# Kernel tuning notes

Hardware: AMD Instinct MI355X
Metric: run time of the kernel (lower is better)

Reference implementation:

```python
import jax, jax.numpy as jnp
import numpy as np

# ---- static config (mirrors init_kwargs) ----
B, T, N, FIN = 32, 12, 500, 2
U, ND, ED = 32, 32, 2            # factor dim, node_dim, edge_dim
NRES, NDIL, NSKIP, NEND, NPRED = 32, 32, 256, 512, 12
NBLOCKS, NLAYERS, KS, ORDER = 4, 2, 2, 2
L = NBLOCKS * NLAYERS
DILATIONS = [2 ** i for _ in range(NBLOCKS) for i in range(NLAYERS)]
RF = NBLOCKS * (KS - 1) * (2 ** NLAYERS - 1) + 1  # receptive field = 13
GCIN = (ORDER * ED + 1) * NDIL                     # graph-conv concat channels = 160
BN_EPS = 1e-5


def conv1x1(x, w, b):
    # x: [B,C,N,T], w: [O,C]
    return jnp.einsum('bcnt,oc->bont', x, w) + b[None, :, None, None]


def dilated_tconv(x, w, b, d):
    # valid dilated conv along time. x: [B,C,N,T], w: [O,C,K]
    k_sz = w.shape[-1]
    t_out = x.shape[-1] - (k_sz - 1) * d
    out = jnp.einsum('bcnt,oc->bont', x[..., 0:t_out], w[..., 0])
    for k in range(1, k_sz):
        out = out + jnp.einsum('bcnt,oc->bont', x[..., k * d:k * d + t_out], w[..., k])
    return out + b[None, :, None, None]


def graph_conv(x, supports, w, b):
    # x: [B,C,N,T]; supports: [E,N,N]; diffusion over node axis (dim 2)
    out = [x]
    for e in range(supports.shape[0]):
        x1 = jnp.einsum('bcvt,vw->bcwt', x, supports[e])
        out.append(x1)
        for _ in range(ORDER - 1):
            x1 = jnp.einsum('bcvt,vw->bcwt', x1, supports[e])
            out.append(x1)
    h = jnp.concatenate(out, axis=1)  # [B,GCIN,N,T]
    return conv1x1(h, w, b)


def batchnorm(x, g, bta):
    m = x.mean(axis=(0, 2, 3), keepdims=True)
    v = ((x - m) ** 2).mean(axis=(0, 2, 3), keepdims=True)
    return (x - m) * jax.lax.rsqrt(v + BN_EPS) * g[None, :, None, None] + bta[None, :, None, None]


def _forward(inputs, factor, map_w, map_b, a1w, a1b, a2w, a2b, a3w, a3b,
             enter_w, enter_b, filt_w, filt_b, gate_w, gate_b,
             skp_w, skp_b, gc_w, gc_b, bn_g, bn_b, o1w, o1b, o2w, o2b):
    n = factor.shape[0]
    # ---- adaptive supports ----
    v = jax.nn.relu(factor @ map_w + map_b)                      # [N, ND]
    src = jnp.broadcast_to(v[None, :, :], (n, n, v.shape[1]))    # src[i,j]=v[j]
    dst = jnp.broadcast_to(v[:, None, :], (n, n, v.shape[1]))    # dst[i,j]=v[i]
    h = jnp.concatenate([src, dst], axis=-1)                     # [N,N,2*ND]
    h = jax.nn.relu(h @ a1w + a1b)
    h = jax.nn.relu(h @ a2w + a2b)
    adj = (h @ a3w + a3b).transpose(2, 0, 1)                     # [E,N,N]
    adj = jax.nn.softmax(adj, axis=2)
    supports = jnp.maximum(adj, jnp.eye(n, dtype=adj.dtype))
    # ---- input split ----
    static = jnp.einsum('btuf,pu->btpf', jnp.einsum('btnf,nu->btuf', inputs, factor), factor)
    x = jnp.concatenate([static, inputs - static], axis=-1)      # [B,T,N,2F]
    x = x.transpose(0, 3, 2, 1)                                  # [B,2F,N,T]
    t_in = x.shape[-1]
    if t_in < RF:
        x = jnp.pad(x, ((0, 0), (0, 0), (0, 0), (RF - t_in, 0)))
    x = conv1x1(x, enter_w, enter_b)                             # [B,NRES,N,RF]
    skip = jnp.zeros((x.shape[0], NSKIP, n, x.shape[-1]), dtype=x.dtype)
    # ---- stacked ST layers ----
    for i, d in enumerate(DILATIONS):
        residual = x
        f = jnp.tanh(dilated_tconv(x, filt_w[i], filt_b[i], d))
        g = jax.nn.sigmoid(dilated_tconv(x, gate_w[i], gate_b[i], d))
        x = f * g                                                # [B,NDIL,N,T']
        s = conv1x1(x, skp_w[i], skp_b[i])
        skip = skip[..., skip.shape[-1] - s.shape[-1]:] + s
        x = graph_conv(x, supports, gc_w[i], gc_b[i])
        x = x + residual[..., residual.shape[-1] - x.shape[-1]:]
        x = batchnorm(x, bn_g[i], bn_b[i])
    # ---- output head ----
    y = jax.nn.relu(skip)
    y = jax.nn.relu(conv1x1(y, o1w, o1b))
    y = conv1x1(y, o2w, o2b)                                     # [B,NPRED,N,1]
    return y, supports


def setup_inputs() -> dict:
    key = jax.random.key(0)
    ks = jax.random.split(key, 16)
    def w(i, shape, s=0.02):
        return s * jax.random.normal(ks[i], shape, dtype=jnp.float32)
    return {
        'inputs': jax.random.normal(ks[0], (B, T, N, FIN), dtype=jnp.float32),
        'factor': 0.05 * jax.random.normal(ks[1], (N, U), dtype=jnp.float32),
        'map_w': w(2, (U, ND), 0.1), 'map_b': jnp.zeros((ND,), jnp.float32),
        'a1w': w(3, (2 * ND, 2 * ND), 0.1), 'a1b': jnp.zeros((2 * ND,), jnp.float32),
        'a2w': w(4, (2 * ND, ND), 0.1), 'a2b': jnp.zeros((ND,), jnp.float32),
        'a3w': w(5, (ND, ED), 0.1), 'a3b': jnp.zeros((ED,), jnp.float32),
        'enter_w': w(6, (NRES, 2 * FIN)), 'enter_b': jnp.zeros((NRES,), jnp.float32),
        'filt_w': w(7, (L, NDIL, NRES, KS)), 'filt_b': jnp.zeros((L, NDIL), jnp.float32),
        'gate_w': w(8, (L, NDIL, NRES, KS)), 'gate_b': jnp.zeros((L, NDIL), jnp.float32),
        'skp_w': w(9, (L, NSKIP, NDIL)), 'skp_b': jnp.zeros((L, NSKIP), jnp.float32),
        'gc_w': w(10, (L, NRES, GCIN)), 'gc_b': jnp.zeros((L, NRES), jnp.float32),
        'bn_g': jnp.ones((L, NRES), jnp.float32), 'bn_b': jnp.zeros((L, NRES), jnp.float32),
        'o1w': w(11, (NEND, NSKIP)), 'o1b': jnp.zeros((NEND,), jnp.float32),
        'o2w': w(12, (NPRED, NEND)), 'o2b': jnp.zeros((NPRED,), jnp.float32),
    }


def reference(inputs, factor, map_w, map_b, a1w, a1b, a2w, a2b, a3w, a3b,
              enter_w, enter_b, filt_w, filt_b, gate_w, gate_b,
              skp_w, skp_b, gc_w, gc_b, bn_g, bn_b, o1w, o1b, o2w, o2b):
    return _forward(inputs, factor, map_w, map_b, a1w, a1b, a2w, a2b, a3w, a3b,
                    enter_w, enter_b, filt_w, filt_b, gate_w, gate_b,
                    skp_w, skp_b, gc_w, gc_b, bn_g, bn_b, o1w, o1b, o2w, o2b)
```

## Files before the change

kernel.cpp:

```cpp
#include <hip/hip_runtime.h>
#include <math.h>

#define BB 32
#define TT 12
#define NN 500
#define UU 32
#define CC 32
#define NSKIPC 256
#define NENDC 512
#define NPREDC 12
#define TX 13
#define TG 12
#define QS 384
#define VS 512
#define BNN (BB*NN)
#define DSZ (BNN*TG*CC)
#define BN_EPS 1e-5f

#define OFF_V      0u
#define OFF_ADJ    16000u
#define OFF_ASRC   516000u
#define OFF_ADST   548000u
#define OFF_PROJ   580000u
#define OFF_STAT   582048u
#define OFF_PART   582560u
#define OFF_BSUM   774560u
#define OFF_X      774816u
#define OFF_XN     7430816u
#define OFF_D      14086816u
#define OFF_GBF    38662816u
#define OFF_GLB    41734816u
#define OFF_GT     43782816u
#define OFF_ST     46928544u
#define OFF_SB     47190688u
#define OFF_ST2    47452832u
#define OFF_WSTB   47714976u
#define OFF_O1WB   47747744u
#define OFF_SKV    47813280u
#define OFF_Y1B    49861280u

typedef __attribute__((ext_vector_type(8))) short bf16x8;
typedef __attribute__((ext_vector_type(4))) float f32x4;

__device__ inline unsigned short f2bf(float f) {
  union { float f; unsigned u; } x; x.f = f;
  unsigned r = x.u + 0x7FFFu + ((x.u >> 16) & 1u);
  return (unsigned short)(r >> 16);
}
__device__ inline float bf2f(short s) {
  union { float f; unsigned u; } x;
  x.u = ((unsigned)(unsigned short)s) << 16;
  return x.f;
}
__device__ inline int pk2(float a, float b) {
  return (int)((unsigned)f2bf(a) | ((unsigned)f2bf(b) << 16));
}
__device__ inline bf16x8 pack8(f32x4 a, f32x4 b) {
  union { int i[4]; bf16x8 v; } u;
  u.i[0]=pk2(a.x,a.y); u.i[1]=pk2(a.z,a.w);
  u.i[2]=pk2(b.x,b.y); u.i[3]=pk2(b.z,b.w);
  return u.v;
}
__device__ inline f32x4 reluadd(f32x4 a, f32x4 b) {
  f32x4 r;
  r.x=fmaxf(a.x+b.x,0.f); r.y=fmaxf(a.y+b.y,0.f);
  r.z=fmaxf(a.z+b.z,0.f); r.w=fmaxf(a.w+b.w,0.f);
  return r;
}


__global__ void k_v(const float* __restrict__ factor, const float* __restrict__ map_w,
                    const float* __restrict__ map_b, float* __restrict__ v) {
  int n = blockIdx.x; int d = threadIdx.x;
  __shared__ float fr[UU];
  fr[d] = factor[n*UU + d];
  __syncthreads();
  float acc = map_b[d];
#pragma unroll
  for (int u=0;u<UU;u++) acc += fr[u]*map_w[u*32+d];
  v[n*32+d] = fmaxf(acc, 0.f);
}

__global__ void k_asrc2(const float* __restrict__ v, const float* __restrict__ a1w,
                        const float* __restrict__ a1b,
                        float* __restrict__ asrc, float* __restrict__ adst) {
  int n = blockIdx.x; int o = threadIdx.x;
  __shared__ float vn[32];
  if (o < 32) vn[o] = v[n*32+o];
  __syncthreads();
  float s = 0.f, dst = a1b[o];
#pragma unroll
  for (int u=0;u<32;u++){ s += vn[u]*a1w[u*64+o]; dst += vn[u]*a1w[(32+u)*64+o]; }
  asrc[n*64+o] = s;
  adst[n*64+o] = dst;
}

__global__ __launch_bounds__(256) void k_pair3(const float* __restrict__ asrc,
    const float* __restrict__ adst, const float* __restrict__ a2w,
    const float* __restrict__ a2b, const float* __restrict__ a3w,
    const float* __restrict__ a3b, float* __restrict__ adj) {
  int i = blockIdx.x;
  int tid = threadIdx.x;
  int wid = tid>>6, lane = tid&63;
  int lm = lane&15, g = lane>>4, lk8 = g*8;
  int jb = blockIdx.y*256 + wid*64;
  bf16x8 wf[2][2];
#pragma unroll
  for (int ks=0;ks<2;ks++)
#pragma unroll
    for (int nh=0;nh<2;nh++){
      int n = nh*16+lm;
      f32x4 lo, hi;
      lo.x=a2w[(ks*32+lk8+0)*32+n]; lo.y=a2w[(ks*32+lk8+1)*32+n];
      lo.z=a2w[(ks*32+lk8+2)*32+n]; lo.w=a2w[(ks*32+lk8+3)*32+n];
      hi.x=a2w[(ks*32+lk8+4)*32+n]; hi.y=a2w[(ks*32+lk8+5)*32+n];
      hi.z=a2w[(ks*32+lk8+6)*32+n]; hi.w=a2w[(ks*32+lk8+7)*32+n];
      wf[ks][nh] = pack8(lo, hi);
    }
  float b20 = a2b[lm], b21 = a2b[16+lm];
  float w3e0n0 = a3w[lm*2],      w3e1n0 = a3w[lm*2+1];
  float w3e0n1 = a3w[(16+lm)*2], w3e1n1 = a3w[(16+lm)*2+1];
  float b30 = a3b[0], b31 = a3b[1];
  const float* dp = adst + i*64;
  f32x4 d00 = *(const f32x4*)(dp + lk8);
  f32x4 d01 = *(const f32x4*)(dp + lk8 + 4);
  f32x4 d10 = *(const f32x4*)(dp + 32 + lk8);
  f32x4 d11 = *(const f32x4*)(dp + 32 + lk8 + 4);
#pragma unroll
  for (int mg=0; mg<4; mg++){
    int j = jb + mg*16 + lm;
    int jc = j < 500 ? j : 0;
    const float* ap = asrc + jc*64;
    f32x4 s00=*(const f32x4*)(ap+lk8),    s01=*(const f32x4*)(ap+lk8+4);
    f32x4 s10=*(const f32x4*)(ap+32+lk8), s11=*(const f32x4*)(ap+32+lk8+4);
    bf16x8 a0 = pack8(reluadd(s00,d00), reluadd(s01,d01));
    bf16x8 a1 = pack8(reluadd(s10,d10), reluadd(s11,d11));
    f32x4 acc0 = {b20,b20,b20,b20};
    f32x4 acc1 = {b21,b21,b21,b21};
    acc0 = __builtin_amdgcn_mfma_f32_16x16x32_bf16(a0, wf[0][0], acc0, 0,0,0);
    acc0 = __builtin_amdgcn_mfma_f32_16x16x32_bf16(a1, wf[1][0], acc0, 0,0,0);
    acc1 = __builtin_amdgcn_mfma_f32_16x16x32_bf16(a0, wf[0][1], acc1, 0,0,0);
    acc1 = __builtin_amdgcn_mfma_f32_16x16x32_bf16(a1, wf[1][1], acc1, 0,0,0);
    float e0[4], e1[4];
#pragma unroll
    for (int r=0;r<4;r++){
      float h2a = fmaxf(acc0[r],0.f), h2b = fmaxf(acc1[r],0.f);
      e0[r] = h2a*w3e0n0 + h2b*w3e0n1;
      e1[r] = h2a*w3e1n0 + h2b*w3e1n1;
    }
#pragma unroll
    for (int off=1; off<16; off<<=1){
#pragma unroll
      for (int r=0;r<4;r++){ e0[r]+=__shfl_xor(e0[r],off); e1[r]+=__shfl_xor(e1[r],off); }
    }
    if (lm==0){
      int j4 = jb + mg*16 + g*4;
      if (j4 < 500){
        f32x4 v0={e0[0]+b30,e0[1]+b30,e0[2]+b30,e0[3]+b30};
        f32x4 v1={e1[0]+b31,e1[1]+b31,e1[2]+b31,e1[3]+b31};
        *(f32x4*)(adj + i*500 + j4) = v0;
        *(f32x4*)(adj + 250000 + i*500 + j4) = v1;
      }
    }
  }
}

__global__ __launch_bounds__(256) void k_softmax(const float* __restrict__ adj,
    float* __restrict__ sup_out) {
  int row = blockIdx.x;
  int e = row/NN, i = row%NN;
  const float* a = adj + e*250000 + i*NN;
  __shared__ float red[64];
  float m = -1e30f;
  for (int j=threadIdx.x;j<NN;j+=256) m = fmaxf(m, a[j]);
#pragma unroll
  for (int off=32; off; off>>=1) m = fmaxf(m, __shfl_down(m, off));
  int lane = threadIdx.x & 63, wid = threadIdx.x >> 6;
  if (lane==0) red[wid]=m;
  __syncthreads();
  if (threadIdx.x==0){ float mm=red[0]; for(int w=1;w<4;w++) mm=fmaxf(mm,red[w]); red[32]=mm; }
  __syncthreads();
  m = red[32];
  float s=0.f;
  for (int j=threadIdx.x;j<NN;j+=256) s += __expf(a[j]-m);
#pragma unroll
  for (int off=32; off; off>>=1) s += __shfl_down(s, off);
  if (lane==0) red[wid]=s;
  __syncthreads();
  if (threadIdx.x==0){ float ss=0; for(int w=0;w<4;w++) ss+=red[w]; red[33]=ss; }
  __syncthreads();
  float inv = 1.f/red[33];
  for (int j=threadIdx.x;j<NN;j+=256) {
    float val = __expf(a[j]-m)*inv;
    if (j==i) val = 1.f;
    sup_out[e*250000 + i*NN + j] = val;
  }
}

__global__ __launch_bounds__(256) void k_tposeS(const float* __restrict__ sup,
    short* __restrict__ ST, short* __restrict__ SB) {
  __shared__ float ts[64][68];
  int e = blockIdx.z;
  int v0 = blockIdx.x*64, w0 = blockIdx.y*64;
  int tid = threadIdx.x;
  int vv = tid>>2, wc = (tid&3)*16;
  bool vok = (v0+vv) < 500;
#pragma unroll
  for (int c=0;c<4;c++){
    f32x4 val = {0,0,0,0};
    int wg = w0 + wc + c*4;
    if (vok && wg < 500) val = *(const f32x4*)(sup + e*250000 + (size_t)(v0+vv)*500 + wg);
    *(f32x4*)&ts[vv][wc + c*4] = val;
    int2 pv; pv.x = pk2(val.x, val.y); pv.y = pk2(val.z, val.w);
    *(int2*)(SB + (size_t)e*(512*512) + (size_t)(v0+vv)*VS + wg) = pv;
  }
  __syncthreads();
  int w = tid>>2, vc = (tid&3)*16;
  unsigned short u[16];
#pragma unroll
  for (int j=0;j<16;j++) u[j] = f2bf(ts[vc+j][w]);
  int4 o0, o1;
  o0.x = u[0]|(u[1]<<16);  o0.y = u[2]|(u[3]<<16);
  o0.z = u[4]|(u[5]<<16);  o0.w = u[6]|(u[7]<<16);
  o1.x = u[8]|(u[9]<<16);  o1.y = u[10]|(u[11]<<16);
  o1.z = u[12]|(u[13]<<16); o1.w = u[14]|(u[15]<<16);
  short* op = ST + (size_t)e*(512*512) + (size_t)(w0+w)*VS + v0 + vc;
  *(int4*)(op) = o0;
  *(int4*)(op+8) = o1;
}

__global__ __launch_bounds__(256) void k_ssq(const short* __restrict__ SB,
    const short* __restrict__ ST, short* __restrict__ ST2) {
  __shared__ __align__(16) short As[64*72];
  __shared__ __align__(16) short Bs[64*72];
  int e = blockIdx.z;
  int u0 = blockIdx.x*64, w0 = blockIdx.y*64;
  const short* Ab = SB + (size_t)e*(512*512);
  const short* Bb = ST + (size_t)e*(512*512);
  int tid = threadIdx.x;
  int row = tid>>2, col = (tid&3)*16;
  const short* ap = Ab + (size_t)(u0+row)*VS + col;
  const short* bp = Bb + (size_t)(w0+row)*VS + col;
  f32x4 ra0 = *(const f32x4*)(ap);
  f32x4 ra1 = *(const f32x4*)(ap+8);
  f32x4 rb0 = *(const f32x4*)(bp);
  f32x4 rb1 = *(const f32x4*)(bp+8);
  int wid = tid>>6, lane = tid&63;
  int wr = wid>>1, wc = wid&1;
  int lm = lane&15, lk = (lane>>4)*8;
  f32x4 acc[2][2] = {};
  short* aw = As + row*72 + col;
  short* bw = Bs + row*72 + col;
  for (int kk=0; kk<8; kk++) {
    __syncthreads();
    *(f32x4*)(aw) = ra0; *(f32x4*)(aw+8) = ra1;
    *(f32x4*)(bw) = rb0; *(f32x4*)(bw+8) = rb1;
    __syncthreads();
    if (kk < 7) {
      const short* ap2 = ap + (kk+1)*64;
      const short* bp2 = bp + (kk+1)*64;
      ra0 = *(const f32x4*)(ap2); ra1 = *(const f32x4*)(ap2+8);
      rb0 = *(const f32x4*)(bp2); rb1 = *(const f32x4*)(bp2+8);
    }
#pragma unroll
    for (int ks=0; ks<2; ks++) {
      bf16x8 af0 = *(const bf16x8*)(As + (wr*32 + lm)*72 + ks*32 + lk);
      bf16x8 af1 = *(const bf16x8*)(As + (wr*32 + 16 + lm)*72 + ks*32 + lk);
      bf16x8 bq0 = *(const bf16x8*)(Bs + (wc*32 + lm)*72 + ks*32 + lk);
      bf16x8 bq1 = *(const bf16x8*)(Bs + (wc*32 + 16 + lm)*72 + ks*32 + lk);
      acc[0][0] = __builtin_amdgcn_mfma_f32_16x16x32_bf16(af0, bq0, acc[0][0], 0,0,0);
      acc[0][1] = __builtin_amdgcn_mfma_f32_16x16x32_bf16(af0, bq1, acc[0][1], 0,0,0);
      acc[1][0] = __builtin_amdgcn_mfma_f32_16x16x32_bf16(af1, bq0, acc[1][0], 0,0,0);
      acc[1][1] = __builtin_amdgcn_mfma_f32_16x16x32_bf16(af1, bq1, acc[1][1], 0,0,0);
    }
  }
#pragma unroll
  for (int fm=0; fm<2; fm++) {
    int u4 = u0 + wr*32 + fm*16 + (lane>>4)*4;
#pragma unroll
    for (int fn=0; fn<2; fn++) {
      int w = w0 + wc*32 + fn*16 + lm;
      f32x4 v4 = acc[fm][fn];
      int2 pv; pv.x = pk2(v4.x, v4.y); pv.y = pk2(v4.z, v4.w);
      *(int2*)(ST2 + (size_t)e*(512*512) + (size_t)w*VS + u4) = pv;
    }
  }
}

__global__ __launch_bounds__(256) void k_tposeGb(const short* __restrict__ Gbf,
    short* __restrict__ GT, int qmax) {
  __shared__ __align__(16) short ts[64][72];
  int b = blockIdx.z;
  int v0 = blockIdx.x*64, q0 = blockIdx.y*64;
  int tid = threadIdx.x;
  int vv = tid>>2, qc = (tid&3)*16;
  bool ok = ((v0+vv) < 500) && ((q0+qc) < qmax);
  int4 z4 = {0,0,0,0};
  int4 i0 = z4, i1 = z4;
  if (ok){
    const short* gp = Gbf + (size_t)(b*NN + v0+vv)*QS + q0 + qc;
    i0 = *(const int4*)(gp);
    i1 = *(const int4*)(gp+8);
  }
  *(int4*)&ts[vv][qc] = i0;
  *(int4*)&ts[vv][qc+8] = i1;
  __syncthreads();
  int q = tid>>2, vc = (tid&3)*16;
  if (q0 + q < qmax) {
    unsigned short u[16];
#pragma unroll
    for (int j=0;j<16;j++) u[j] = (unsigned short)ts[vc+j][q];
    int4 o0, o1;
    o0.x = u[0]|(u[1]<<16);  o0.y = u[2]|(u[3]<<16);
    o0.z = u[4]|(u[5]<<16);  o0.w = u[6]|(u[7]<<16);
    o1.x = u[8]|(u[9]<<16);  o1.y = u[10]|(u[11]<<16);
    o1.z = u[12]|(u[13]<<16); o1.w = u[14]|(u[15]<<16);
    short* op = GT + ((size_t)b*QS + q0+q)*VS + v0 + vc;
    *(int4*)(op) = o0;
    *(int4*)(op+8) = o1;
  }
}

__global__ __launch_bounds__(256) void k_hop(const short* __restrict__ ST,
    const short* __restrict__ ST2, const short* __restrict__ GT,
    short* __restrict__ Dout, int qmax) {
  __shared__ __align__(16) short As[64*72];
  __shared__ __align__(16) short Bs[64*72];
  int sel = blockIdx.z & 3, b = blockIdx.z >> 2;
  int e = sel >> 1, hop = sel & 1;
  int w0 = blockIdx.x*64, q0 = blockIdx.y*64;
  const short* Ab = (hop ? ST2 : ST) + (size_t)e*(512*512);
  const short* Bb = GT + (size_t)b*(QS*VS);
  int tid = threadIdx.x;
  int row = tid>>2, col = (tid&3)*16;
  const short* ap = Ab + (size_t)(w0+row)*VS + col;
  const short* bp = Bb + (size_t)(q0+row)*VS + col;
  bool bok = (q0+row) < qmax;
  f32x4 zero4 = {0,0,0,0};
  f32x4 ra0 = *(const f32x4*)(ap);
  f32x4 ra1 = *(const f32x4*)(ap+8);
  f32x4 rb0 = bok ? *(const f32x4*)(bp) : zero4;
  f32x4 rb1 = bok ? *(const f32x4*)(bp+8) : zero4;
  int wid = tid>>6, lane = tid&63;
  int wr = wid>>1, wc = wid&1;
  int lm = lane&15, lk = (lane>>4)*8;
  f32x4 acc[2][2] = {};
  short* aw = As + row*72 + col;
  short* bw = Bs + row*72 + col;
  for (int kk=0; kk<8; kk++) {
    __syncthreads();
    *(f32x4*)(aw) = ra0; *(f32x4*)(aw+8) = ra1;
    *(f32x4*)(bw) = rb0; *(f32x4*)(bw+8) = rb1;
    __syncthreads();
    if (kk < 7) {
      const short* ap2 = ap + (kk+1)*64;
      const short* bp2 = bp + (kk+1)*64;
      ra0 = *(const f32x4*)(ap2); ra1 = *(const f32x4*)(ap2+8);
      rb0 = bok ? *(const f32x4*)(bp2) : zero4;
      rb1 = bok ? *(const f32x4*)(bp2+8) : zero4;
    }
#pragma unroll
    for (int ks=0; ks<2; ks++) {
      bf16x8 af0 = *(const bf16x8*)(As + (wr*32 + lm)*72 + ks*32 + lk);
      bf16x8 af1 = *(const bf16x8*)(As + (wr*32 + 16 + lm)*72 + ks*32 + lk);
      bf16x8 bq0 = *(const bf16x8*)(Bs + (wc*32 + lm)*72 + ks*32 + lk);
      bf16x8 bq1 = *(const bf16x8*)(Bs + (wc*32 + 16 + lm)*72 + ks*32 + lk);
      acc[0][0] = __builtin_amdgcn_mfma_f32_16x16x32_bf16(af0, bq0, acc[0][0], 0,0,0);
      acc[0][1] = __builtin_amdgcn_mfma_f32_16x16x32_bf16(af0, bq1, acc[0][1], 0,0,0);
      acc[1][0] = __builtin_amdgcn_mfma_f32_16x16x32_bf16(af1, bq0, acc[1][0], 0,0,0);
      acc[1][1] = __builtin_amdgcn_mfma_f32_16x16x32_bf16(af1, bq1, acc[1][1], 0,0,0);
    }
  }
  short* Ob = Dout + (size_t)sel*DSZ + (size_t)b*(NN*QS);
#pragma unroll
  for (int fm=0; fm<2; fm++) {
    int wb4 = w0 + wr*32 + fm*16 + (lane>>4)*4;
    if (wb4 >= 500) continue;
#pragma unroll
    for (int fn=0; fn<2; fn++) {
      int q = q0 + wc*32 + fn*16 + lm;
      if (q < qmax) {
        f32x4 v4 = acc[fm][fn];
        short* op = Ob + (size_t)wb4*QS + q;
        op[0*QS] = (short)f2bf(v4.x);
        op[1*QS] = (short)f2bf(v4.y);
        op[2*QS] = (short)f2bf(v4.z);
        op[3*QS] = (short)f2bf(v4.w);
      }
    }
  }
}


__global__ void k_proj(const float* __restrict__ inputs, const float* __restrict__ factor,
                       float* __restrict__ proj) {
  int bt = blockIdx.x;
  __shared__ float xin[NN*2];
  for (int idx=threadIdx.x; idx<NN*2; idx+=64) xin[idx] = inputs[bt*NN*2 + idx];
  __syncthreads();
  int u = threadIdx.x>>1, f = threadIdx.x&1;
  float acc=0.f;
  for (int n=0;n<NN;n++) acc += xin[n*2+f]*factor[n*UU+u];
  proj[bt*64 + u*2+f] = acc;
}

__global__ __launch_bounds__(256) void k_enter(const float* __restrict__ inputs,
    const float* __restrict__ factor, const float* __restrict__ proj,
    const float* __restrict__ ew, const float* __restrict__ eb, float* __restrict__ X) {
  int idx = blockIdx.x*256+threadIdx.x;
  if (idx >= BB*NN*TX) return;
  int t = idx % TX; int n = (idx/TX)%NN; int b = idx/(TX*NN);
  float x4[4]={0.f,0.f,0.f,0.f};
  if (t>0) {
    int tt=t-1;
    float s0=0.f,s1=0.f;
    const float* pr = proj + (b*TT+tt)*64;
    const float* fr = factor + n*UU;
#pragma unroll
    for(int u=0;u<UU;u++){ s0 += pr[u*2]*fr[u]; s1 += pr[u*2+1]*fr[u]; }
    float i0 = inputs[((b*TT+tt)*NN+n)*2];
    float i1 = inputs[((b*TT+tt)*NN+n)*2+1];
    x4[0]=s0; x4[1]=s1; x4[2]=i0-s0; x4[3]=i1-s1;
  }
  float* xp = X + ((size_t)(b*NN+n)*TX + t)*CC;
#pragma unroll
  for(int o=0;o<CC;o++){
    xp[o] = eb[o] + ew[o*4]*x4[0] + ew[o*4+1]*x4[1] + ew[o*4+2]*x4[2] + ew[o*4+3]*x4[3];
  }
}


__global__ __launch_bounds__(256) void k_gated3(const float* __restrict__ X,
    short* __restrict__ Gbf, short* __restrict__ Glb,
    const float* __restrict__ fw, const float* __restrict__ fb,
    const float* __restrict__ gw, const float* __restrict__ gb,
    const float* __restrict__ stat, int use_stat, int d, int t_out, int lidx) {
  __shared__ __align__(16) short As[64*72];
  __shared__ __align__(16) short Wb[64*72];
  __shared__ float scs[32], shs[32];
  int tid = threadIdx.x;
  if (tid < 32) {
    scs[tid] = use_stat ? stat[tid] : 1.0f;
    shs[tid] = use_stat ? stat[32 + tid] : 0.0f;
  }
  for (int i = tid; i < 2048; i += 256) {
    int o = i >> 6, k = i & 63;
    Wb[o*72 + k]      = (short)f2bf(fw[i]);
    Wb[(32+o)*72 + k] = (short)f2bf(gw[i]);
  }
  __syncthreads();
  int m0 = blockIdx.x * 64;
  {
    int mm = tid & 63;
    int kb = (tid >> 6) * 16;
    int c0 = kb >> 1;
    int m = m0 + mm;
    int bn = m / t_out, t = m - bn * t_out;
    const float* xr = X + (size_t)bn * (TX * CC);
    float4 a0 = *(const float4*)(xr + t * 32 + c0);
    float4 a1 = *(const float4*)(xr + t * 32 + c0 + 4);
    float4 b0 = *(const float4*)(xr + (t + d) * 32 + c0);
    float4 b1 = *(const float4*)(xr + (t + d) * 32 + c0 + 4);
    float va[8] = {a0.x,a0.y,a0.z,a0.w,a1.x,a1.y,a1.z,a1.w};
    float vb[8] = {b0.x,b0.y,b0.z,b0.w,b1.x,b1.y,b1.z,b1.w};
    int iv[8];
#pragma unroll
    for (int j = 0; j < 8; j++) {
      float sc = scs[c0+j], sh = shs[c0+j];
      iv[j] = pk2(va[j]*sc + sh, vb[j]*sc + sh);
    }
    int4 w0 = {iv[0],iv[1],iv[2],iv[3]};
    int4 w1 = {iv[4],iv[5],iv[6],iv[7]};
    *(int4*)(As + mm*72 + kb) = w0;
    *(int4*)(As + mm*72 + kb + 8) = w1;
  }
  __syncthreads();
  int wid = tid>>6, lane = tid&63;
  int lm = lane&15, g = lane>>4, lk8 = g*8;
  f32x4 acc[4] = {};
#pragma unroll
  for (int kk=0; kk<2; kk++){
    bf16x8 af = *(const bf16x8*)(As + (wid*16+lm)*72 + kk*32 + lk8);
#pragma unroll
    for (int fn=0; fn<4; fn++){
      bf16x8 bq = *(const bf16x8*)(Wb + (fn*16+lm)*72 + kk*32 + lk8);
      acc[fn] = __builtin_amdgcn_mfma_f32_16x16x32_bf16(af, bq, acc[fn], 0,0,0);
    }
  }
#pragma unroll
  for (int fn=0; fn<2; fn++){
    int o = fn*16 + lm;
    float fbv = fb[o], gbv = gb[o];
#pragma unroll
    for (int r=0; r<4; r++){
      int m = m0 + wid*16 + g*4 + r;
      int bn = m / t_out, t = m - bn*t_out;
      float f = acc[fn][r] + fbv;
      float gg = acc[fn+2][r] + gbv;
      float th = 2.f/(1.f+__expf(-2.f*f)) - 1.f;
      float sg = 1.f/(1.f+__expf(-gg));
      unsigned short ov = f2bf(th*sg);
      Gbf[(size_t)bn*QS + t*32 + o] = (short)ov;
      if (t == t_out-1) Glb[(size_t)bn*256 + lidx*32 + o] = (short)ov;
    }
  }
}


template<int TOUT>
__global__ __launch_bounds__(64) void k_gc3(const short* __restrict__ Gbf,
    const short* __restrict__ Dbf, const float* __restrict__ Xc, float* __restrict__ Xn,
    const float* __restrict__ gcw, const float* __restrict__ gcb,
    const float* __restrict__ stat, int use_stat, float* __restrict__ part, int d) {
  int tid = threadIdx.x;
  int lm = tid&15, g = tid>>4, lk8 = g*8;
  bf16x8 wf[5][2];
#pragma unroll
  for (int ks=0;ks<5;ks++)
#pragma unroll
    for (int nh=0;nh<2;nh++){
      const float* wp = gcw + (nh*16+lm)*160 + ks*32 + lk8;
      wf[ks][nh] = pack8(*(const f32x4*)wp, *(const f32x4*)(wp+4));
    }
  float scn0 = use_stat ? stat[lm]    : 1.f;
  float scn1 = use_stat ? stat[16+lm] : 1.f;
  float shn0 = use_stat ? stat[32+lm] : 0.f;
  float shn1 = use_stat ? stat[48+lm] : 0.f;
  float gb0 = gcb[lm], gb1 = gcb[16+lm];
  int m0 = blockIdx.x*64;
  float ss0=0.f, sq0=0.f, ss1=0.f, sq1=0.f;
#pragma unroll
  for (int mg=0; mg<4; mg++){
    int m = m0 + mg*16 + lm;
    int bn = m / TOUT; int t = m - bn*TOUT;
    size_t off = (size_t)bn*(TG*CC) + t*32 + lk8;
    f32x4 acc0={0,0,0,0}, acc1={0,0,0,0};
    {
      bf16x8 af = *(const bf16x8*)(Gbf + off);
      acc0 = __builtin_amdgcn_mfma_f32_16x16x32_bf16(af, wf[0][0], acc0, 0,0,0);
      acc1 = __builtin_amdgcn_mfma_f32_16x16x32_bf16(af, wf[0][1], acc1, 0,0,0);
    }
#pragma unroll
    for (int ks=1;ks<5;ks++){
      bf16x8 af = *(const bf16x8*)(Dbf + (size_t)(ks-1)*DSZ + off);
      acc0 = __builtin_amdgcn_mfma_f32_16x16x32_bf16(af, wf[ks][0], acc0, 0,0,0);
      acc1 = __builtin_amdgcn_mfma_f32_16x16x32_bf16(af, wf[ks][1], acc1, 0,0,0);
    }
#pragma unroll
    for (int r=0;r<4;r++){
      int mr = m0 + mg*16 + g*4 + r;
      int bnr = mr / TOUT; int tr = mr - bnr*TOUT;
      size_t xoff = (size_t)bnr*(TX*CC);
      float r0 = Xc[xoff + (tr+d)*32 + lm];
      float r1 = Xc[xoff + (tr+d)*32 + 16 + lm];
      float v0 = acc0[r] + gb0 + r0*scn0 + shn0;
      float v1 = acc1[r] + gb1 + r1*scn1 + shn1;
      Xn[xoff + tr*32 + lm] = v0;
      Xn[xoff + tr*32 + 16 + lm] = v1;
      ss0+=v0; sq0+=v0*v0; ss1+=v1; sq1+=v1*v1;
    }
  }
#pragma unroll
  for (int off=16; off<64; off<<=1){
    ss0+=__shfl_xor(ss0,off); sq0+=__shfl_xor(sq0,off);
    ss1+=__shfl_xor(ss1,off); sq1+=__shfl_xor(sq1,off);
  }
  if (tid<16){
    float* pp = part + (size_t)blockIdx.x*64;
    pp[tid]=ss0; pp[16+tid]=ss1; pp[32+tid]=sq0; pp[48+tid]=sq1;
  }
}

__global__ __launch_bounds__(64) void k_stat2a(const float* __restrict__ part, int nblk,
    float* __restrict__ part2) {
  int t = threadIdx.x;
  float s = 0.f;
  for (int i = blockIdx.x; i < nblk; i += 64) s += part[(size_t)i*64 + t];
  part2[blockIdx.x*64 + t] = s;
}

__global__ __launch_bounds__(64) void k_stat2b(const float* __restrict__ part2,
    const float* __restrict__ g, const float* __restrict__ b,
    float* __restrict__ statout, float cntinv) {
  int t = threadIdx.x;
  float s = 0.f;
#pragma unroll 8
  for (int i = 0; i < 64; i++) s += part2[i*64 + t];
  __shared__ float red[64];
  red[t] = s;
  __syncthreads();
  if (t < 32){
    float sum = red[t], sq = red[32+t];
    float m = sum*cntinv, var = sq*cntinv - m*m;
    float sc = rsqrtf(var + BN_EPS)*g[t];
    statout[t] = sc;
    statout[32+t] = b[t] - m*sc;
  }
}


__global__ void k_wstack2(const float* __restrict__ skp_w, const float* __restrict__ skp_b,
                          const float* __restrict__ o1w,
                          short* __restrict__ Wstb, short* __restrict__ o1wb,
                          float* __restrict__ bsum) {
  int bid = blockIdx.x;
  int idx = bid*256 + threadIdx.x;
  if (bid < 256){
    int kk = idx >> 8, o = idx & 255;
    Wstb[o*256 + kk] = (short)f2bf(skp_w[(kk>>5)*8192 + o*32 + (kk&31)]);
    if (idx < 256){
      float s=0.f;
      for (int l=0;l<8;l++) s += skp_b[l*256+idx];
      bsum[idx]=s;
    }
  } else {
    int j = idx - 65536;
    o1wb[j] = (short)f2bf(o1w[j]);
  }
}

__global__ __launch_bounds__(256) void k_mm(const short* __restrict__ A,
    const short* __restrict__ B, const float* __restrict__ bias,
    short* __restrict__ out, int ldout, int K) {
  __shared__ __align__(16) short As[64*72];
  __shared__ __align__(16) short Bs[64*72];
  int m0 = blockIdx.x*64, n0 = blockIdx.y*64;
  int tid = threadIdx.x;
  int row = tid>>2, col = (tid&3)*16;
  const short* ap = A + (size_t)(m0+row)*K + col;
  const short* bp = B + (size_t)(n0+row)*K + col;
  f32x4 ra0 = *(const f32x4*)(ap);
  f32x4 ra1 = *(const f32x4*)(ap+8);
  f32x4 rb0 = *(const f32x4*)(bp);
  f32x4 rb1 = *(const f32x4*)(bp+8);
  int wid = tid>>6, lane = tid&63;
  int wr = wid>>1, wc = wid&1;
  int lm = lane&15, lk = (lane>>4)*8;
  f32x4 acc[2][2] = {};
  short* aw = As + row*72 + col;
  short* bw = Bs + row*72 + col;
  int nk = K>>6;
  for (int kk=0; kk<nk; kk++) {
    __syncthreads();
    *(f32x4*)(aw) = ra0; *(f32x4*)(aw+8) = ra1;
    *(f32x4*)(bw) = rb0; *(f32x4*)(bw+8) = rb1;
    __syncthreads();
    if (kk < nk-1) {
      const short* ap2 = ap + (kk+1)*64;
      const short* bp2 = bp + (kk+1)*64;
      ra0 = *(const f32x4*)(ap2); ra1 = *(const f32x4*)(ap2+8);
      rb0 = *(const f32x4*)(bp2); rb1 = *(const f32x4*)(bp2+8);
    }
#pragma unroll
    for (int ks=0; ks<2; ks++) {
      bf16x8 af0 = *(const bf16x8*)(As + (wr*32 + lm)*72 + ks*32 + lk);
      bf16x8 af1 = *(const bf16x8*)(As + (wr*32 + 16 + lm)*72 + ks*32 + lk);
      bf16x8 bq0 = *(const bf16x8*)(Bs + (wc*32 + lm)*72 + ks*32 + lk);
      bf16x8 bq1 = *(const bf16x8*)(Bs + (wc*32 + 16 + lm)*72 + ks*32 + lk);
      acc[0][0] = __builtin_amdgcn_mfma_f32_16x16x32_bf16(af0, bq0, acc[0][0], 0,0,0);
      acc[0][1] = __builtin_amdgcn_mfma_f32_16x16x32_bf16(af0, bq1, acc[0][1], 0,0,0);
      acc[1][0] = __builtin_amdgcn_mfma_f32_16x16x32_bf16(af1, bq0, acc[1][0], 0,0,0);
      acc[1][1] = __builtin_amdgcn_mfma_f32_16x16x32_bf16(af1, bq1, acc[1][1], 0,0,0);
    }
  }
#pragma unroll
  for (int fm=0; fm<2; fm++) {
    int mb = m0 + wr*32 + fm*16 + (lane>>4)*4;
#pragma unroll
    for (int fn=0; fn<2; fn++) {
      int n = n0 + wc*32 + fn*16 + lm;
      float bv = bias[n];
      f32x4 v4 = acc[fm][fn];
#pragma unroll
      for (int r=0;r<4;r++)
        out[(size_t)(mb+r)*ldout + n] = (short)f2bf(fmaxf(v4[r]+bv, 0.f));
    }
  }
}

__global__ __launch_bounds__(256) void k_head2c(const short* __restrict__ Y1b,
    const float* __restrict__ o2w, const float* __restrict__ o2b, float* __restrict__ y) {
  int tid = threadIdx.x;
  int ml = tid>>2, kc = tid&3;
  int m = blockIdx.x*64 + ml;
  float accs[NPREDC] = {};
  for (int e=kc*128; e<kc*128+128; e+=8){
    bf16x8 yv = *(const bf16x8*)(Y1b + (size_t)m*NENDC + e);
    float yf[8];
#pragma unroll
    for (int j=0;j<8;j++) yf[j] = bf2f(yv[j]);
#pragma unroll
    for (int p=0;p<NPREDC;p++){
      const float* wp = o2w + p*NENDC + e;
      float a = 0.f;
#pragma unroll
      for (int j=0;j<8;j++) a += wp[j]*yf[j];
      accs[p] += a;
    }
  }
#pragma unroll
  for (int off=1; off<4; off<<=1)
#pragma unroll
    for (int p=0;p<NPREDC;p++) accs[p] += __shfl_xor(accs[p], off);
  if (kc==0){
    int b=m/NN, n=m%NN;
#pragma unroll
    for (int p=0;p<NPREDC;p++) y[(b*NPREDC+p)*NN+n] = accs[p] + o2b[p];
  }
}


extern "C" void kernel_launch(void* const* d_in, const int* in_sizes, int n_in,
                              void* d_out, int out_size, void* d_ws, size_t ws_size,
                              hipStream_t stream) {
  const float* inputs  = (const float*)d_in[0];
  const float* factor  = (const float*)d_in[1];
  const float* map_w   = (const float*)d_in[2];
  const float* map_b   = (const float*)d_in[3];
  const float* a1w     = (const float*)d_in[4];
  const float* a1b     = (const float*)d_in[5];
  const float* a2w     = (const float*)d_in[6];
  const float* a2b     = (const float*)d_in[7];
  const float* a3w     = (const float*)d_in[8];
  const float* a3b     = (const float*)d_in[9];
  const float* enter_w = (const float*)d_in[10];
  const float* enter_b = (const float*)d_in[11];
  const float* filt_w  = (const float*)d_in[12];
  const float* filt_b  = (const float*)d_in[13];
  const float* gate_w  = (const float*)d_in[14];
  const float* gate_b  = (const float*)d_in[15];
  const float* skp_w   = (const float*)d_in[16];
  const float* skp_b   = (const float*)d_in[17];
  const float* gc_w    = (const float*)d_in[18];
  const float* gc_b    = (const float*)d_in[19];
  const float* bn_g    = (const float*)d_in[20];
  const float* bn_b    = (const float*)d_in[21];
  const float* o1w     = (const float*)d_in[22];
  const float* o1b     = (const float*)d_in[23];
  const float* o2w     = (const float*)d_in[24];
  const float* o2b     = (const float*)d_in[25];
  (void)in_sizes; (void)n_in; (void)out_size; (void)ws_size;

  float* ws = (float*)d_ws;
  float* v      = ws + OFF_V;
  float* adj    = ws + OFF_ADJ;
  float* part2  = ws + OFF_ADJ;
  float* asrc   = ws + OFF_ASRC;
  float* adst   = ws + OFF_ADST;
  float* proj   = ws + OFF_PROJ;
  float* statb  = ws + OFF_STAT;
  float* part   = ws + OFF_PART;
  float* bsum   = ws + OFF_BSUM;
  float* X      = ws + OFF_X;
  float* Xn     = ws + OFF_XN;
  short* Dbf    = (short*)(ws + OFF_D);
  short* Gbf    = (short*)(ws + OFF_GBF);
  short* Glb    = (short*)(ws + OFF_GLB);
  short* GT     = (short*)(ws + OFF_GT);
  short* ST     = (short*)(ws + OFF_ST);
  short* SB     = (short*)(ws + OFF_SB);
  short* ST2    = (short*)(ws + OFF_ST2);
  short* Wstb   = (short*)(ws + OFF_WSTB);
  short* o1wb   = (short*)(ws + OFF_O1WB);
  short* skvb   = (short*)(ws + OFF_SKV);
  short* Y1b    = (short*)(ws + OFF_Y1B);

  float* y_out   = (float*)d_out;
  float* sup_out = y_out + BB*NPREDC*NN;

  k_v<<<NN, 32, 0, stream>>>(factor, map_w, map_b, v);
  k_asrc2<<<NN, 64, 0, stream>>>(v, a1w, a1b, asrc, adst);
  {
    dim3 gp(NN, 2);
    k_pair3<<<gp, 256, 0, stream>>>(asrc, adst, a2w, a2b, a3w, a3b, adj);
  }
  k_softmax<<<2*NN, 256, 0, stream>>>(adj, sup_out);
  {
    dim3 gt(8, 8, 2);
    k_tposeS<<<gt, 256, 0, stream>>>(sup_out, ST, SB);
    k_ssq<<<gt, 256, 0, stream>>>(SB, ST, ST2);
  }

  k_proj<<<BB*TT, 64, 0, stream>>>(inputs, factor, proj);
  k_enter<<<(BB*NN*TX+255)/256, 256, 0, stream>>>(inputs, factor, proj, enter_w, enter_b, X);

  k_wstack2<<<768, 256, 0, stream>>>(skp_w, skp_b, o1w, Wstb, o1wb, bsum);

  float* Xc = X; float* Xo = Xn;
  int t = TX;
  static const int dil[8]={1,2,1,2,1,2,1,2};
  for (int l=0;l<7;l++){
    int d=dil[l], t_out=t-d;
    const float* st = statb + (l>0 ? (l-1)*64 : 0);
    k_gated3<<<250*t_out,256,0,stream>>>(Xc, Gbf, Glb, filt_w + l*2048, filt_b + l*32,
                                         gate_w + l*2048, gate_b + l*32, st, l>0, d, t_out, l);
    int qmax = t_out*CC;
    int qt = (qmax+63)/64;
    dim3 gtp(8, qt, 32);
    k_tposeGb<<<gtp,256,0,stream>>>(Gbf, GT, qmax);
    dim3 ghp(8, qt, 128);
    k_hop<<<ghp,256,0,stream>>>(ST, ST2, GT, Dbf, qmax);
    int nblk = 250*t_out;
    const float* gcwl = gc_w + l*5120;
    const float* gcbl = gc_b + l*32;
    switch (t_out){
      case 12: k_gc3<12><<<nblk,64,0,stream>>>(Gbf,Dbf,Xc,Xo,gcwl,gcbl,st,l>0,part,d); break;
      case 10: k_gc3<10><<<nblk,64,0,stream>>>(Gbf,Dbf,Xc,Xo,gcwl,gcbl,st,l>0,part,d); break;
      case  9: k_gc3< 9><<<nblk,64,0,stream>>>(Gbf,Dbf,Xc,Xo,gcwl,gcbl,st,l>0,part,d); break;
      case  7: k_gc3< 7><<<nblk,64,0,stream>>>(Gbf,Dbf,Xc,Xo,gcwl,gcbl,st,l>0,part,d); break;
      case  6: k_gc3< 6><<<nblk,64,0,stream>>>(Gbf,Dbf,Xc,Xo,gcwl,gcbl,st,l>0,part,d); break;
      case  4: k_gc3< 4><<<nblk,64,0,stream>>>(Gbf,Dbf,Xc,Xo,gcwl,gcbl,st,l>0,part,d); break;
      default: k_gc3< 3><<<nblk,64,0,stream>>>(Gbf,Dbf,Xc,Xo,gcwl,gcbl,st,l>0,part,d); break;
    }
    k_stat2a<<<64,64,0,stream>>>(part, nblk, part2);
    k_stat2b<<<1,64,0,stream>>>(part2, bn_g + l*32, bn_b + l*32,
                                statb + l*64, 1.f/(16000.f*(float)t_out));
    float* tmp=Xc; Xc=Xo; Xo=tmp;
    t = t_out;
  }
  k_gated3<<<250*1,256,0,stream>>>(Xc, Gbf, Glb, filt_w + 7*2048, filt_b + 7*32,
                                   gate_w + 7*2048, gate_b + 7*32, statb + 6*64, 1, 2, 1, 7);

  {
    dim3 gs(BNN/64, NSKIPC/64);
    k_mm<<<gs,256,0,stream>>>(Glb, Wstb, bsum, skvb, NSKIPC, 256);
    dim3 gh(BNN/64, NENDC/64);
    k_mm<<<gh,256,0,stream>>>(skvb, o1wb, o1b, Y1b, NENDC, 256);
    k_head2c<<<BNN/64,256,0,stream>>>(Y1b, o2w, o2b, y_out);
  }
}
```

Baseline: 792.3 us.

## Enlarge hop GEMM tiles to 128x128 and pack four waves per gc block

The diffusion hop GEMM now uses 128x128 output tiles, with each wave computing a 4x4 grid of MFMA fragments. This raises arithmetic intensity and reduces redundant global and LDS loads of the support and feature tiles. The graph-conv output kernel now runs four independent waves per 256-thread block, and partial stats are indexed per wave, with zeroed slots for out-of-range waves. Costs are higher register and LDS use per block, fewer blocks for the hop GEMM, and some unmasked reads of padded rows beyond qmax.

```diff
diff --git a/kernel.cpp b/kernel.cpp
--- a/kernel.cpp
+++ b/kernel.cpp
@@ -321,64 +321,68 @@
   }
 }
 
-__global__ __launch_bounds__(256) void k_hop(const short* __restrict__ ST,
+__global__ __launch_bounds__(256) void k_hop2(const short* __restrict__ ST,
     const short* __restrict__ ST2, const short* __restrict__ GT,
     short* __restrict__ Dout, int qmax) {
-  __shared__ __align__(16) short As[64*72];
-  __shared__ __align__(16) short Bs[64*72];
+  __shared__ __align__(16) short As[128*72];
+  __shared__ __align__(16) short Bs[128*72];
   int sel = blockIdx.z & 3, b = blockIdx.z >> 2;
   int e = sel >> 1, hop = sel & 1;
-  int w0 = blockIdx.x*64, q0 = blockIdx.y*64;
-  const short* Ab = (hop ? ST2 : ST) + (size_t)e*(512*512);
-  const short* Bb = GT + (size_t)b*(QS*VS);
+  int w0 = blockIdx.x*128, q0 = blockIdx.y*128;
+  const short* Ab = (hop ? ST2 : ST) + (size_t)e*(512*512) + (size_t)w0*VS;
+  const short* Bb = GT + (size_t)b*(QS*VS) + (size_t)q0*VS;
   int tid = threadIdx.x;
   int row = tid>>2, col = (tid&3)*16;
-  const short* ap = Ab + (size_t)(w0+row)*VS + col;
-  const short* bp = Bb + (size_t)(q0+row)*VS + col;
-  bool bok = (q0+row) < qmax;
-  f32x4 zero4 = {0,0,0,0};
-  f32x4 ra0 = *(const f32x4*)(ap);
-  f32x4 ra1 = *(const f32x4*)(ap+8);
-  f32x4 rb0 = bok ? *(const f32x4*)(bp) : zero4;
-  f32x4 rb1 = bok ? *(const f32x4*)(bp+8) : zero4;
+  const short* ap0 = Ab + (size_t)row*VS + col;
+  const short* ap1 = ap0 + (size_t)64*VS;
+  const short* bp0 = Bb + (size_t)row*VS + col;
+  const short* bp1 = bp0 + (size_t)64*VS;
+  f32x4 a00=*(const f32x4*)ap0, a01=*(const f32x4*)(ap0+8);
+  f32x4 a10=*(const f32x4*)ap1, a11=*(const f32x4*)(ap1+8);
+  f32x4 b00=*(const f32x4*)bp0, b01=*(const f32x4*)(bp0+8);
+  f32x4 b10=*(const f32x4*)bp1, b11=*(const f32x4*)(bp1+8);
   int wid = tid>>6, lane = tid&63;
   int wr = wid>>1, wc = wid&1;
   int lm = lane&15, lk = (lane>>4)*8;
-  f32x4 acc[2][2] = {};
-  short* aw = As + row*72 + col;
-  short* bw = Bs + row*72 + col;
+  f32x4 acc[4][4] = {};
+  short* aw0 = As + row*72 + col; short* aw1 = aw0 + 64*72;
+  short* bw0 = Bs + row*72 + col; short* bw1 = bw0 + 64*72;
   for (int kk=0; kk<8; kk++) {
     __syncthreads();
-    *(f32x4*)(aw) = ra0; *(f32x4*)(aw+8) = ra1;
-    *(f32x4*)(bw) = rb0; *(f32x4*)(bw+8) = rb1;
+    *(f32x4*)(aw0) = a00; *(f32x4*)(aw0+8) = a01;
+    *(f32x4*)(aw1) = a10; *(f32x4*)(aw1+8) = a11;
+    *(f32x4*)(bw0) = b00; *(f32x4*)(bw0+8) = b01;
+    *(f32x4*)(bw1) = b10; *(f32x4*)(bw1+8) = b11;
     __syncthreads();
     if (kk < 7) {
-      const short* ap2 = ap + (kk+1)*64;
-      const short* bp2 = bp + (kk+1)*64;
-      ra0 = *(const f32x4*)(ap2); ra1 = *(const f32x4*)(ap2+8);
-      rb0 = bok ? *(const f32x4*)(bp2) : zero4;
-      rb1 = bok ? *(const f32x4*)(bp2+8) : zero4;
+      int o = (kk+1)*64;
+      a00=*(const f32x4*)(ap0+o); a01=*(const f32x4*)(ap0+o+8);
+      a10=*(const f32x4*)(ap1+o); a11=*(const f32x4*)(ap1+o+8);
+      b00=*(const f32x4*)(bp0+o); b01=*(const f32x4*)(bp0+o+8);
+      b10=*(const f32x4*)(bp1+o); b11=*(const f32x4*)(bp1+o+8);
     }
 #pragma unroll
     for (int ks=0; ks<2; ks++) {
-      bf16x8 af0 = *(const bf16x8*)(As + (wr*32 + lm)*72 + ks*32 + lk);
-      bf16x8 af1 = *(const bf16x8*)(As + (wr*32 + 16 + lm)*72 + ks*32 + lk);
-      bf16x8 bq0 = *(const bf16x8*)(Bs + (wc*32 + lm)*72 + ks*32 + lk);
-      bf16x8 bq1 = *(const bf16x8*)(Bs + (wc*32 + 16 + lm)*72 + ks*32 + lk);
-      acc[0][0] = __builtin_amdgcn_mfma_f32_16x16x32_bf16(af0, bq0, acc[0][0], 0,0,0);
-      acc[0][1] = __builtin_amdgcn_mfma_f32_16x16x32_bf16(af0, bq1, acc[0][1], 0,0,0);
-      acc[1][0] = __builtin_amdgcn_mfma_f32_16x16x32_bf16(af1, bq0, acc[1][0], 0,0,0);
-      acc[1][1] = __builtin_amdgcn_mfma_f32_16x16x32_bf16(af1, bq1, acc[1][1], 0,0,0);
+      bf16x8 af[4], bq[4];
+#pragma unroll
+      for (int fm=0;fm<4;fm++) af[fm] = *(const bf16x8*)(As + (wr*64+fm*16+lm)*72 + ks*32 + lk);
+#pragma unroll
+      for (int fn=0;fn<4;fn++) bq[fn] = *(const bf16x8*)(Bs + (wc*64+fn*16+lm)*72 + ks*32 + lk);
+#pragma unroll
+      for (int fm=0;fm<4;fm++)
+#pragma unroll
+        for (int fn=0;fn<4;fn++)
+          acc[fm][fn] = __builtin_amdgcn_mfma_f32_16x16x32_bf16(af[fm], bq[fn], acc[fm][fn], 0,0,0);
     }
   }
   short* Ob = Dout + (size_t)sel*DSZ + (size_t)b*(NN*QS);
 #pragma unroll
-  for (int fm=0; fm<2; fm++) {
-    int wb4 = w0 + wr*32 + fm*16 + (lane>>4)*4;
+  for (int fm=0; fm<4; fm++) {
+    int wb4 = w0 + wr*64 + fm*16 + (lane>>4)*4;
     if (wb4 >= 500) continue;
 #pragma unroll
-    for (int fn=0; fn<2; fn++) {
-      int q = q0 + wc*32 + fn*16 + lm;
+    for (int fn=0; fn<4; fn++) {
+      int q = q0 + wc*64 + fn*16 + lm;
       if (q < qmax) {
         f32x4 v4 = acc[fm][fn];
         short* op = Ob + (size_t)wb4*QS + q;
@@ -508,12 +512,20 @@
 
 
 template<int TOUT>
-__global__ __launch_bounds__(64) void k_gc3(const short* __restrict__ Gbf,
+__global__ __launch_bounds__(256) void k_gc3(const short* __restrict__ Gbf,
     const short* __restrict__ Dbf, const float* __restrict__ Xc, float* __restrict__ Xn,
     const float* __restrict__ gcw, const float* __restrict__ gcb,
     const float* __restrict__ stat, int use_stat, float* __restrict__ part, int d) {
   int tid = threadIdx.x;
-  int lm = tid&15, g = tid>>4, lk8 = g*8;
+  int wid = tid>>6, lane = tid&63;
+  int lm = lane&15, g = lane>>4, lk8 = g*8;
+  int m0 = blockIdx.x*256 + wid*64;
+  const int M = 16000*TOUT;
+  float* pp = part + ((size_t)blockIdx.x*4 + wid)*64;
+  if (m0 >= M){
+    if (lane < 16){ pp[lane]=0.f; pp[16+lane]=0.f; pp[32+lane]=0.f; pp[48+lane]=0.f; }
+    return;
+  }
   bf16x8 wf[5][2];
 #pragma unroll
   for (int ks=0;ks<5;ks++)
@@ -527,7 +539,6 @@
   float shn0 = use_stat ? stat[32+lm] : 0.f;
   float shn1 = use_stat ? stat[48+lm] : 0.f;
   float gb0 = gcb[lm], gb1 = gcb[16+lm];
-  int m0 = blockIdx.x*64;
   float ss0=0.f, sq0=0.f, ss1=0.f, sq1=0.f;
 #pragma unroll
   for (int mg=0; mg<4; mg++){
@@ -565,9 +576,8 @@
     ss0+=__shfl_xor(ss0,off); sq0+=__shfl_xor(sq0,off);
     ss1+=__shfl_xor(ss1,off); sq1+=__shfl_xor(sq1,off);
   }
-  if (tid<16){
-    float* pp = part + (size_t)blockIdx.x*64;
-    pp[tid]=ss0; pp[16+tid]=ss1; pp[32+tid]=sq0; pp[48+tid]=sq1;
+  if (lane<16){
+    pp[lane]=ss0; pp[16+lane]=ss1; pp[32+lane]=sq0; pp[48+lane]=sq1;
   }
 }
 
@@ -795,24 +805,25 @@
     k_gated3<<<250*t_out,256,0,stream>>>(Xc, Gbf, Glb, filt_w + l*2048, filt_b + l*32,
                                          gate_w + l*2048, gate_b + l*32, st, l>0, d, t_out, l);
     int qmax = t_out*CC;
-    int qt = (qmax+63)/64;
-    dim3 gtp(8, qt, 32);
+    int qt64 = (qmax+63)/64;
+    dim3 gtp(8, qt64, 32);
     k_tposeGb<<<gtp,256,0,stream>>>(Gbf, GT, qmax);
-    dim3 ghp(8, qt, 128);
-    k_hop<<<ghp,256,0,stream>>>(ST, ST2, GT, Dbf, qmax);
-    int nblk = 250*t_out;
+    int qt128 = (qmax+127)/128;
+    dim3 ghp(4, qt128, 128);
+    k_hop2<<<ghp,256,0,stream>>>(ST, ST2, GT, Dbf, qmax);
+    int nb = (16000*t_out + 255)/256;
     const float* gcwl = gc_w + l*5120;
     const float* gcbl = gc_b + l*32;
     switch (t_out){
-      case 12: k_gc3<12><<<nblk,64,0,stream>>>(Gbf,Dbf,Xc,Xo,gcwl,gcbl,st,l>0,part,d); break;
-      case 10: k_gc3<10><<<nblk,64,0,stream>>>(Gbf,Dbf,Xc,Xo,gcwl,gcbl,st,l>0,part,d); break;
-      case  9: k_gc3< 9><<<nblk,64,0,stream>>>(Gbf,Dbf,Xc,Xo,gcwl,gcbl,st,l>0,part,d); break;
-      case  7: k_gc3< 7><<<nblk,64,0,stream>>>(Gbf,Dbf,Xc,Xo,gcwl,gcbl,st,l>0,part,d); break;
-      case  6: k_gc3< 6><<<nblk,64,0,stream>>>(Gbf,Dbf,Xc,Xo,gcwl,gcbl,st,l>0,part,d); break;
-      case  4: k_gc3< 4><<<nblk,64,0,stream>>>(Gbf,Dbf,Xc,Xo,gcwl,gcbl,st,l>0,part,d); break;
-      default: k_gc3< 3><<<nblk,64,0,stream>>>(Gbf,Dbf,Xc,Xo,gcwl,gcbl,st,l>0,part,d); break;
-    }
-    k_stat2a<<<64,64,0,stream>>>(part, nblk, part2);
+      case 12: k_gc3<12><<<nb,256,0,stream>>>(Gbf,Dbf,Xc,Xo,gcwl,gcbl,st,l>0,part,d); break;
+      case 10: k_gc3<10><<<nb,256,0,stream>>>(Gbf,Dbf,Xc,Xo,gcwl,gcbl,st,l>0,part,d); break;
+      case  9: k_gc3< 9><<<nb,256,0,stream>>>(Gbf,Dbf,Xc,Xo,gcwl,gcbl,st,l>0,part,d); break;
+      case  7: k_gc3< 7><<<nb,256,0,stream>>>(Gbf,Dbf,Xc,Xo,gcwl,gcbl,st,l>0,part,d); break;
+      case  6: k_gc3< 6><<<nb,256,0,stream>>>(Gbf,Dbf,Xc,Xo,gcwl,gcbl,st,l>0,part,d); break;
+      case  4: k_gc3< 4><<<nb,256,0,stream>>>(Gbf,Dbf,Xc,Xo,gcwl,gcbl,st,l>0,part,d); break;
+      default: k_gc3< 3><<<nb,256,0,stream>>>(Gbf,Dbf,Xc,Xo,gcwl,gcbl,st,l>0,part,d); break;
+    }
+    k_stat2a<<<64,64,0,stream>>>(part, nb*4, part2);
     k_stat2b<<<1,64,0,stream>>>(part2, bn_g + l*32, bn_b + l*32,
                                 statb + l*64, 1.f/(16000.f*(float)t_out));
     float* tmp=Xc; Xc=Xo; Xo=tmp;
```

Result: faster. 771.4 us (-2.6%).
